# Performance work log

Hardware: AMD Instinct MI355X
Metric: run time of the kernel (lower is better)

The kernel has to match this reference:

```python
import jax, jax.numpy as jnp
import numpy as np
from jax import lax

B, L, F, H, K = 16, 512, 384, 384, 3
MAX_OUT = 4096  # static upper bound on sum of durations (L * (fill_max-1) = 3584)
EPS = 1e-5
PAD = K // 2


def setup_inputs() -> dict:
    key = jax.random.key(0)
    ks = jax.random.split(key, 6)
    s = 0.02
    return {
        "input": jax.random.normal(ks[0], (B, L, F), jnp.float32),
        "target": jax.random.randint(ks[1], (B, L), 0, 8, jnp.int32),
        "conv1_w": jax.random.normal(ks[2], (H, F, K), jnp.float32) * s,
        "conv1_b": jnp.zeros((H,), jnp.float32),
        "ln1_g": jnp.ones((H,), jnp.float32),
        "ln1_b": jnp.zeros((H,), jnp.float32),
        "conv2_w": jax.random.normal(ks[3], (F, H, K), jnp.float32) * s,
        "conv2_b": jnp.zeros((F,), jnp.float32),
        "ln2_g": jnp.ones((F,), jnp.float32),
        "ln2_b": jnp.zeros((F,), jnp.float32),
        "lin_w": jax.random.normal(ks[4], (F, 1), jnp.float32) * s,
        "lin_b": jnp.zeros((1,), jnp.float32),
    }


def _conv1d(x, w, b):
    # x: [B, L, Cin] -> [B, L, Cout]; w: [Cout, Cin, K] (torch Conv1d layout)
    y = lax.conv_general_dilated(
        x.transpose(0, 2, 1), w, window_strides=(1,), padding=[(PAD, PAD)],
        dimension_numbers=("NCH", "OIH", "NCH"))
    return y.transpose(0, 2, 1) + b


def _layer_norm(x, g, b):
    mu = jnp.mean(x, axis=-1, keepdims=True)
    var = jnp.mean(jnp.square(x - mu), axis=-1, keepdims=True)
    return (x - mu) * lax.rsqrt(var + EPS) * g + b


def _length_regulate(x, dur_int):
    # cumsum-based index mapping + gather (vectorized LR_function)
    ends = jnp.cumsum(dur_int, axis=-1)                      # [B, L]
    ts = jnp.arange(MAX_OUT)                                 # [T]
    idx = jax.vmap(lambda e: jnp.searchsorted(e, ts, side="right"))(ends)  # [B, T]
    gathered = jnp.take_along_axis(x, jnp.clip(idx, 0, L - 1)[:, :, None], axis=1)
    mask = (ts[None, :] < ends[:, -1:]).astype(x.dtype)      # zero-pad past total length
    return gathered * mask[:, :, None]


def reference(input, target, conv1_w, conv1_b, ln1_g, ln1_b,
              conv2_w, conv2_b, ln2_g, ln2_b, lin_w, lin_b):
    # DurationPredictor (eval mode: dropout is identity)
    h = jax.nn.relu(_layer_norm(_conv1d(input, conv1_w, conv1_b), ln1_g, ln1_b))
    h = jax.nn.relu(_layer_norm(_conv1d(h, conv2_w, conv2_b), ln2_g, ln2_b))
    durations = jnp.exp(jax.nn.relu(h @ lin_w + lin_b))       # [B, L, 1]
    # LR_function with target durations (round of int target is identity)
    out = _length_regulate(input, target)                      # [B, MAX_OUT, F]
    return out, durations
```

## Files before the change

kernel.cpp:

```cpp
#include <hip/hip_runtime.h>
#include <math.h>

#define B_ 16
#define L_ 512
#define F_ 384
#define H_ 384
#define K_ 3
#define MAX_OUT_ 4096
#define EPS_ 1e-5f

#define M_TOTAL (B_ * L_)
#define KDIM (K_ * F_)
#define NMB 128
#define NCG 6
#define NST 36
#define APANEL (66 * 64)
#define AMBLK (12 * APANEL)
#define APLANE (NMB * AMBLK)
#define BSTEP 4096
#define BCG (NST * BSTEP)
#define BPLANE (NCG * BCG)

typedef __attribute__((ext_vector_type(8))) short bf16x8;
typedef __attribute__((ext_vector_type(4))) float f32x4;

__device__ inline unsigned short bf16_rne(float v) {
    unsigned int u = __float_as_uint(v);
    unsigned int r = (u + 0x7fffu + ((u >> 16) & 1u)) >> 16;
    return (unsigned short)r;
}
__device__ inline void bf16_split(float v, unsigned short& hi, unsigned short& lo) {
    hi = bf16_rne(v);
    float hf = __uint_as_float(((unsigned int)hi) << 16);
    lo = bf16_rne(v - hf);
}

__global__ void k_scan_idx(const int* __restrict__ target, int* __restrict__ idx) {
    __shared__ int e[L_];
    const int b = blockIdx.x;
    const int tid = threadIdx.x;
    e[tid] = target[b * L_ + tid];
    __syncthreads();
    for (int off = 1; off < L_; off <<= 1) {
        int add = (tid >= off) ? e[tid - off] : 0;
        __syncthreads();
        e[tid] += add;
        __syncthreads();
    }
    const int total = e[L_ - 1];
    for (int t = tid; t < MAX_OUT_; t += L_) {
        int lo = 0, hi = L_;
        while (lo < hi) {
            int m = (lo + hi) >> 1;
            if (e[m] <= t) lo = m + 1; else hi = m;
        }
        int v = (t < total) ? min(lo, L_ - 1) : -1;
        idx[b * MAX_OUT_ + t] = v;
    }
}

__global__ void k_prep(const float* __restrict__ x,
                       const float* __restrict__ w1, const float* __restrict__ w2,
                       unsigned short* __restrict__ aph, unsigned short* __restrict__ apl,
                       unsigned short* __restrict__ b1h, unsigned short* __restrict__ b1l,
                       unsigned short* __restrict__ b2h, unsigned short* __restrict__ b2l) {
    const int NA8 = NMB * 12 * 66 * 4;
    const int NB8 = NCG * NST * 64 * 4;
    const int total = NA8 + 2 * NB8;
    for (int i = blockIdx.x * blockDim.x + threadIdx.x; i < total;
         i += gridDim.x * blockDim.x) {
        if (i < NA8) {
            const int m = i / 3168;
            int r1 = i - m * 3168;
            const int fs = r1 / 264;
            int r2 = r1 - fs * 264;
            const int rp = r2 >> 2;
            const int p = r2 & 3;
            const int cgk = p ^ ((rp >> 1) & 3);
            const int f0 = fs * 32 + cgk * 8;
            const int ll = ((m & 7) << 6) + rp - 1;
            ushort4 h0 = {0,0,0,0}, h1 = {0,0,0,0}, l0 = {0,0,0,0}, l1 = {0,0,0,0};
            if (ll >= 0 && ll < L_) {
                const float* src = x + ((size_t)((m >> 3) * L_ + ll) * F_ + f0);
                float4 va = ((const float4*)src)[0];
                float4 vb = ((const float4*)src)[1];
                bf16_split(va.x, h0.x, l0.x); bf16_split(va.y, h0.y, l0.y);
                bf16_split(va.z, h0.z, l0.z); bf16_split(va.w, h0.w, l0.w);
                bf16_split(vb.x, h1.x, l1.x); bf16_split(vb.y, h1.y, l1.y);
                bf16_split(vb.z, h1.z, l1.z); bf16_split(vb.w, h1.w, l1.w);
            }
            ((ushort4*)aph)[i * 2] = h0;  ((ushort4*)aph)[i * 2 + 1] = h1;
            ((ushort4*)apl)[i * 2] = l0;  ((ushort4*)apl)[i * 2 + 1] = l1;
        } else {
            int j = i - NA8;
            const int conv = j / NB8;
            int j2 = j - conv * NB8;
            const float* w = conv ? w2 : w1;
            unsigned short* bh = conv ? b2h : b1h;
            unsigned short* bl = conv ? b2l : b1l;
            const int cg = j2 / 9216;
            int r1 = j2 - cg * 9216;
            const int s = r1 / 256;
            int r2 = r1 - s * 256;
            const int rc = r2 >> 2;
            const int p = r2 & 3;
            const int tap = s / 12;
            const int fs = s - tap * 12;
            const int cgk = p ^ ((rc >> 1) & 3);
            const int f0 = fs * 32 + cgk * 8;
            const int h = cg * 64 + rc;
            ushort4 hv0, hv1, lv0, lv1;
            unsigned short th, tl;
#define WSPLIT(E, DH, DL) bf16_split(w[(size_t)(h * F_ + f0 + (E)) * K_ + tap], th, tl); DH = th; DL = tl;
            WSPLIT(0, hv0.x, lv0.x) WSPLIT(1, hv0.y, lv0.y)
            WSPLIT(2, hv0.z, lv0.z) WSPLIT(3, hv0.w, lv0.w)
            WSPLIT(4, hv1.x, lv1.x) WSPLIT(5, hv1.y, lv1.y)
            WSPLIT(6, hv1.z, lv1.z) WSPLIT(7, hv1.w, lv1.w)
#undef WSPLIT
            ((ushort4*)bh)[j2 * 2] = hv0;  ((ushort4*)bh)[j2 * 2 + 1] = hv1;
            ((ushort4*)bl)[j2 * 2] = lv0;  ((ushort4*)bl)[j2 * 2 + 1] = lv1;
        }
    }
}

typedef __attribute__((address_space(3))) char lds_char;
typedef const __attribute__((address_space(1))) char g_char;

#define GLDS(gsrc, ldst)                                                   \
    __builtin_amdgcn_global_load_lds((g_char*)(gsrc), (lds_char*)(ldst), 16, 0, 0)

#define ST(S) {                                                            \
    const int off = wvA ? ((((S) % 12) * 66 + (S) / 12) * 64) : ((S) * 4096); \
    _Pragma("unroll")                                                      \
    for (int q = 0; q < 4; ++q)                                            \
        GLDS(srcbase + off + q * 1024,                                     \
             smem + ((S) % 3) * 16384 + wvoff + q * 1024);                 \
}

#define MFMA1(A, Bv, MI, NI)                                               \
    acc[MI][NI] = __builtin_amdgcn_mfma_f32_16x16x32_bf16(A, Bv, acc[MI][NI], 0, 0, 0);

#define STEP(S, NW, DOSTAGE) {                                             \
    asm volatile("s_waitcnt vmcnt(" #NW ")" ::: "memory");                 \
    __builtin_amdgcn_s_barrier();                                          \
    const char* bb = smem + ((S) % 3) * 16384;                             \
    const int tp = (S) / 12;                                               \
    bf16x8 ah0 = *(const bf16x8*)(bb + aadr0[tp]);                         \
    bf16x8 ah1 = *(const bf16x8*)(bb + aadr1[tp]);                         \
    bf16x8 al0 = *(const bf16x8*)(bb + 4096 + aadr0[tp]);                  \
    bf16x8 al1 = *(const bf16x8*)(bb + 4096 + aadr1[tp]);                  \
    bf16x8 bh0 = *(const bf16x8*)(bb + 8192 + badr0);                      \
    bf16x8 bh1 = *(const bf16x8*)(bb + 8192 + badr1);                      \
    bf16x8 bl0 = *(const bf16x8*)(bb + 12288 + badr0);                     \
    bf16x8 bl1 = *(const bf16x8*)(bb + 12288 + badr1);                     \
    asm volatile("s_waitcnt lgkmcnt(0)" ::: "memory");                     \
    __builtin_amdgcn_sched_barrier(0);                                     \
    __builtin_amdgcn_s_barrier();                                          \
    DOSTAGE;                                                               \
    __builtin_amdgcn_s_setprio(1);                                         \
    MFMA1(ah0, bh0, 0, 0) MFMA1(ah0, bh1, 0, 1)                            \
    MFMA1(ah1, bh0, 1, 0) MFMA1(ah1, bh1, 1, 1)                            \
    MFMA1(ah0, bl0, 0, 0) MFMA1(ah0, bl1, 0, 1)                            \
    MFMA1(ah1, bl0, 1, 0) MFMA1(ah1, bl1, 1, 1)                            \
    MFMA1(al0, bh0, 0, 0) MFMA1(al0, bh1, 0, 1)                            \
    MFMA1(al1, bh0, 1, 0) MFMA1(al1, bh1, 1, 1)                            \
    __builtin_amdgcn_s_setprio(0);                                         \
}

__global__ __launch_bounds__(256, 3) void k_gemm(
        const unsigned short* __restrict__ Aph,
        const unsigned short* __restrict__ Apl,
        const unsigned short* __restrict__ Bph,
        const unsigned short* __restrict__ Bpl,
        float* __restrict__ C) {
    __shared__ __align__(1024) char smem[49152];
    const int lane = threadIdx.x & 63;
    const int wv = threadIdx.x >> 6;
    const int wr = wv >> 1;
    const int wc = wv & 1;
    const int m = blockIdx.x;
    const int cg = blockIdx.y;
    const int r0 = m * 64;
    const int h0 = cg * 64;

    const bool wvA = (wv < 2);
    const int wvoff = wv * 4096;
    const char* srcbase;
    {
        const char* ap = (wv == 0) ? (const char*)Aph : (const char*)Apl;
        const char* bp = (wv == 2) ? (const char*)Bph : (const char*)Bpl;
        srcbase = (wvA ? ap + (size_t)m * AMBLK : bp + (size_t)cg * BCG) + lane * 16;
    }

    const int fr = lane & 15;
    const int fc = lane >> 4;
    const int rowA0 = wr * 32 + fr, rowA1 = rowA0 + 16;
    const int colB0 = wc * 32 + fr, colB1 = colB0 + 16;
    int aadr0[3], aadr1[3];
#pragma unroll
    for (int t = 0; t < 3; ++t) {
        aadr0[t] = rowA0 * 64 + ((fc ^ (((rowA0 + t) >> 1) & 3)) << 4);
        aadr1[t] = rowA1 * 64 + ((fc ^ (((rowA1 + t) >> 1) & 3)) << 4);
    }
    const int badr0 = colB0 * 64 + ((fc ^ ((colB0 >> 1) & 3)) << 4);
    const int badr1 = colB1 * 64 + ((fc ^ ((colB1 >> 1) & 3)) << 4);

    const f32x4 z4 = {0.f, 0.f, 0.f, 0.f};
    f32x4 acc[2][2];
    acc[0][0] = z4; acc[0][1] = z4; acc[1][0] = z4; acc[1][1] = z4;

    ST(0) ST(1) ST(2)

    STEP(0, 8, ST(3))   STEP(1, 8, ST(4))   STEP(2, 8, ST(5))
    STEP(3, 8, ST(6))   STEP(4, 8, ST(7))   STEP(5, 8, ST(8))
    STEP(6, 8, ST(9))   STEP(7, 8, ST(10))  STEP(8, 8, ST(11))
    STEP(9, 8, ST(12))  STEP(10, 8, ST(13)) STEP(11, 8, ST(14))
    STEP(12, 8, ST(15)) STEP(13, 8, ST(16)) STEP(14, 8, ST(17))
    STEP(15, 8, ST(18)) STEP(16, 8, ST(19)) STEP(17, 8, ST(20))
    STEP(18, 8, ST(21)) STEP(19, 8, ST(22)) STEP(20, 8, ST(23))
    STEP(21, 8, ST(24)) STEP(22, 8, ST(25)) STEP(23, 8, ST(26))
    STEP(24, 8, ST(27)) STEP(25, 8, ST(28)) STEP(26, 8, ST(29))
    STEP(27, 8, ST(30)) STEP(28, 8, ST(31)) STEP(29, 8, ST(32))
    STEP(30, 8, ST(33)) STEP(31, 8, ST(34)) STEP(32, 8, ST(35))
    STEP(33, 8, )       STEP(34, 4, )       STEP(35, 0, )

    const int rb = (lane >> 4) * 4;
#pragma unroll
    for (int mi = 0; mi < 2; ++mi)
#pragma unroll
        for (int ni = 0; ni < 2; ++ni)
#pragma unroll
            for (int r = 0; r < 4; ++r)
                C[(size_t)(r0 + wr * 32 + mi * 16 + rb + r) * H_ +
                  h0 + wc * 32 + ni * 16 + fr] = acc[mi][ni][r];
}

__global__ __launch_bounds__(256) void k_lnrelu(
        const float* __restrict__ c, const float* __restrict__ cb,
        const float* __restrict__ g, const float* __restrict__ bt,
        unsigned short* __restrict__ oh, unsigned short* __restrict__ ol) {
    const int row = blockIdx.x * 4 + (threadIdx.x >> 6);
    const int lane = threadIdx.x & 63;
    const float* cr = c + (size_t)row * H_;
    float2 dv[3];
    dv[0] = ((const float2*)cr)[lane];
    dv[1] = ((const float2*)cr)[lane + 64];
    dv[2] = ((const float2*)cr)[lane + 128];
#pragma unroll
    for (int p = 0; p < 3; ++p) {
        const int ch = 2 * (lane + 64 * p);
        dv[p].x += cb[ch];
        dv[p].y += cb[ch + 1];
    }
    float s = dv[0].x + dv[0].y + dv[1].x + dv[1].y + dv[2].x + dv[2].y;
    float s2 = dv[0].x * dv[0].x + dv[0].y * dv[0].y + dv[1].x * dv[1].x
             + dv[1].y * dv[1].y + dv[2].x * dv[2].x + dv[2].y * dv[2].y;
    for (int off = 32; off >= 1; off >>= 1) {
        s += __shfl_xor(s, off);
        s2 += __shfl_xor(s2, off);
    }
    const float mu = s * (1.f / H_);
    const float var = s2 * (1.f / H_) - mu * mu;
    const float rs = rsqrtf(var + EPS_);
    unsigned short hv[6], lv[6];
#pragma unroll
    for (int p = 0; p < 3; ++p) {
        const int ch = 2 * (lane + 64 * p);
        float r0 = fmaxf((dv[p].x - mu) * rs * g[ch] + bt[ch], 0.f);
        float r1 = fmaxf((dv[p].y - mu) * rs * g[ch + 1] + bt[ch + 1], 0.f);
        bf16_split(r0, hv[2 * p], lv[2 * p]);
        bf16_split(r1, hv[2 * p + 1], lv[2 * p + 1]);
    }
#define WSLOT(M, RP) {                                                        \
    _Pragma("unroll")                                                         \
    for (int p = 0; p < 3; ++p) {                                             \
        const int ch = 2 * (lane + 64 * p);                                   \
        const int fs = ch >> 5;                                               \
        const int k32 = ch & 31;                                              \
        const int pst = (k32 >> 3) ^ (((RP) >> 1) & 3);                       \
        const size_t ix = ((size_t)(((M) * 12 + fs) * 66 + (RP)) * 4 + pst) * 8 + (k32 & 7); \
        *(ushort2*)(oh + ix) = make_ushort2(hv[2 * p], hv[2 * p + 1]);        \
        *(ushort2*)(ol + ix) = make_ushort2(lv[2 * p], lv[2 * p + 1]);        \
    }                                                                         \
}
    const int m1 = row >> 6;
    const int rsub = row & 63;
    WSLOT(m1, rsub + 1);
    if (rsub == 0 && (row & 511) != 0)   WSLOT(m1 - 1, 65);
    if (rsub == 63 && (row & 511) != 511) WSLOT(m1 + 1, 0);
#undef WSLOT
}

__global__ __launch_bounds__(256) void k_fin(
        const float* __restrict__ c, const float* __restrict__ cb,
        const float* __restrict__ g, const float* __restrict__ bt,
        const float* __restrict__ lw, const float* __restrict__ lb,
        float* __restrict__ dur) {
    const int row = blockIdx.x * 4 + (threadIdx.x >> 6);
    const int lane = threadIdx.x & 63;
    const float* cr = c + (size_t)row * F_;
    float2 dv[3];
    dv[0] = ((const float2*)cr)[lane];
    dv[1] = ((const float2*)cr)[lane + 64];
    dv[2] = ((const float2*)cr)[lane + 128];
#pragma unroll
    for (int p = 0; p < 3; ++p) {
        const int ch = 2 * (lane + 64 * p);
        dv[p].x += cb[ch];
        dv[p].y += cb[ch + 1];
    }
    float s = dv[0].x + dv[0].y + dv[1].x + dv[1].y + dv[2].x + dv[2].y;
    float s2 = dv[0].x * dv[0].x + dv[0].y * dv[0].y + dv[1].x * dv[1].x
             + dv[1].y * dv[1].y + dv[2].x * dv[2].x + dv[2].y * dv[2].y;
    for (int off = 32; off >= 1; off >>= 1) {
        s += __shfl_xor(s, off);
        s2 += __shfl_xor(s2, off);
    }
    const float mu = s * (1.f / F_);
    const float var = s2 * (1.f / F_) - mu * mu;
    const float rs = rsqrtf(var + EPS_);
    float dot = 0.f;
#pragma unroll
    for (int p = 0; p < 3; ++p) {
        const int ch = 2 * (lane + 64 * p);
        float r0 = fmaxf((dv[p].x - mu) * rs * g[ch] + bt[ch], 0.f);
        float r1 = fmaxf((dv[p].y - mu) * rs * g[ch + 1] + bt[ch + 1], 0.f);
        dot += r0 * lw[ch] + r1 * lw[ch + 1];
    }
    for (int off = 32; off >= 1; off >>= 1) dot += __shfl_xor(dot, off);
    if (lane == 0) dur[row] = expf(fmaxf(dot + lb[0], 0.f));
}

__global__ void k_gather(const float4* __restrict__ x, const int* __restrict__ idx,
                         float4* __restrict__ out) {
    const int F4 = F_ / 4;
    const int total = B_ * MAX_OUT_ * F4;
    for (int i = blockIdx.x * blockDim.x + threadIdx.x; i < total;
         i += gridDim.x * blockDim.x) {
        int row = i / F4;
        int f4 = i - row * F4;
        int t = row % MAX_OUT_;
        int b = row / MAX_OUT_;
        int id = idx[b * MAX_OUT_ + t];
        float4 v = make_float4(0.f, 0.f, 0.f, 0.f);
        if (id >= 0) v = x[((size_t)b * L_ + id) * F4 + f4];
        out[i] = v;
    }
}

extern "C" void kernel_launch(void* const* d_in, const int* in_sizes, int n_in,
                              void* d_out, int out_size, void* d_ws, size_t ws_size,
                              hipStream_t stream) {
    const float* input   = (const float*)d_in[0];
    const int*   target  = (const int*)d_in[1];
    const float* conv1_w = (const float*)d_in[2];
    const float* conv1_b = (const float*)d_in[3];
    const float* ln1_g   = (const float*)d_in[4];
    const float* ln1_b   = (const float*)d_in[5];
    const float* conv2_w = (const float*)d_in[6];
    const float* conv2_b = (const float*)d_in[7];
    const float* ln2_g   = (const float*)d_in[8];
    const float* ln2_b   = (const float*)d_in[9];
    const float* lin_w   = (const float*)d_in[10];
    const float* lin_b   = (const float*)d_in[11];

    float* out0 = (float*)d_out;
    float* dur  = out0 + (size_t)B_ * MAX_OUT_ * F_;
    float* c    = out0;
    char* ob = (char*)d_out;
    unsigned short* aph = (unsigned short*)(ob + (16u << 20));
    unsigned short* apl = (unsigned short*)(ob + (24u << 20));

    char* ws = (char*)d_ws;
    int* idx = (int*)ws;
    unsigned short* b1h = (unsigned short*)(ws + 262144);
    unsigned short* b1l = b1h + BPLANE / 2;
    unsigned short* b2h = b1l + BPLANE / 2;
    unsigned short* b2l = b2h + BPLANE / 2;

    hipLaunchKernelGGL(k_scan_idx, dim3(B_), dim3(L_), 0, stream, target, idx);
    hipLaunchKernelGGL(k_prep, dim3(2048), dim3(256), 0, stream,
                       input, conv1_w, conv2_w, aph, apl, b1h, b1l, b2h, b2l);
    hipLaunchKernelGGL(k_gemm, dim3(NMB, NCG), dim3(256), 0, stream,
                       aph, apl, b1h, b1l, c);
    hipLaunchKernelGGL(k_lnrelu, dim3(M_TOTAL / 4), dim3(256), 0, stream,
                       c, conv1_b, ln1_g, ln1_b, aph, apl);
    hipLaunchKernelGGL(k_gemm, dim3(NMB, NCG), dim3(256), 0, stream,
                       aph, apl, b2h, b2l, c);
    hipLaunchKernelGGL(k_fin, dim3(M_TOTAL / 4), dim3(256), 0, stream,
                       c, conv2_b, ln2_g, ln2_b, lin_w, lin_b, dur);
    hipLaunchKernelGGL(k_gather, dim3(4096), dim3(256), 0, stream,
                       (const float4*)input, idx, (float4*)out0);
}
```

Measured before the change: 101.8 us.

## Load GEMM B operand directly into registers with double-buffered prefetch

The B (weight) fragments are no longer staged through LDS. Each wave loads its B fragments straight from global memory into registers, prefetching one stage ahead with alternating X/Y register sets. All four waves now share the A-tile staging through LDS, two async global-to-LDS loads each, which halves the shared-memory footprint and removes LDS traffic for B. In exchange it adds register pressure and relies on global/L2 latency for the B loads, with hand-tuned vmcnt wait counts that must match the new mix of outstanding loads.

```diff
diff --git a/kernel.cpp b/kernel.cpp
--- a/kernel.cpp
+++ b/kernel.cpp
@@ -130,40 +130,44 @@
     __builtin_amdgcn_global_load_lds((g_char*)(gsrc), (lds_char*)(ldst), 16, 0, 0)
 
 #define ST(S) {                                                            \
-    const int off = wvA ? ((((S) % 12) * 66 + (S) / 12) * 64) : ((S) * 4096); \
-    _Pragma("unroll")                                                      \
-    for (int q = 0; q < 4; ++q)                                            \
-        GLDS(srcbase + off + q * 1024,                                     \
-             smem + ((S) % 3) * 16384 + wvoff + q * 1024);                 \
+    const int offp = (((S) % 12) * 66 + (S) / 12) * 64;                    \
+    GLDS(asrc0 + offp, smem + ((S) % 3) * 8192 + dst0);                    \
+    GLDS(asrc1 + offp, smem + ((S) % 3) * 8192 + dst1);                    \
+}
+
+#define LDB(S, R) {                                                        \
+    R##h0 = *(const bf16x8*)(bsrch + (S) * 4096 + badr0);                  \
+    R##h1 = *(const bf16x8*)(bsrch + (S) * 4096 + badr1);                  \
+    R##l0 = *(const bf16x8*)(bsrcl + (S) * 4096 + badr0);                  \
+    R##l1 = *(const bf16x8*)(bsrcl + (S) * 4096 + badr1);                  \
 }
 
 #define MFMA1(A, Bv, MI, NI)                                               \
     acc[MI][NI] = __builtin_amdgcn_mfma_f32_16x16x32_bf16(A, Bv, acc[MI][NI], 0, 0, 0);
 
-#define STEP(S, NW, DOSTAGE) {                                             \
-    asm volatile("s_waitcnt vmcnt(" #NW ")" ::: "memory");                 \
+#define SB __builtin_amdgcn_sched_barrier(0)
+
+#define STEP(S, KA, DOST, DOLDB, BH0, BH1, BL0, BL1) {                     \
+    asm volatile("s_waitcnt vmcnt(" #KA ")" ::: "memory");                 \
     __builtin_amdgcn_s_barrier();                                          \
-    const char* bb = smem + ((S) % 3) * 16384;                             \
-    const int tp = (S) / 12;                                               \
-    bf16x8 ah0 = *(const bf16x8*)(bb + aadr0[tp]);                         \
-    bf16x8 ah1 = *(const bf16x8*)(bb + aadr1[tp]);                         \
-    bf16x8 al0 = *(const bf16x8*)(bb + 4096 + aadr0[tp]);                  \
-    bf16x8 al1 = *(const bf16x8*)(bb + 4096 + aadr1[tp]);                  \
-    bf16x8 bh0 = *(const bf16x8*)(bb + 8192 + badr0);                      \
-    bf16x8 bh1 = *(const bf16x8*)(bb + 8192 + badr1);                      \
-    bf16x8 bl0 = *(const bf16x8*)(bb + 12288 + badr0);                     \
-    bf16x8 bl1 = *(const bf16x8*)(bb + 12288 + badr1);                     \
+    const char* bb = smem + ((S) % 3) * 8192;                              \
+    bf16x8 ah0 = *(const bf16x8*)(bb + aadr0[(S) / 12]);                   \
+    bf16x8 ah1 = *(const bf16x8*)(bb + aadr1[(S) / 12]);                   \
+    bf16x8 al0 = *(const bf16x8*)(bb + 4096 + aadr0[(S) / 12]);            \
+    bf16x8 al1 = *(const bf16x8*)(bb + 4096 + aadr1[(S) / 12]);            \
     asm volatile("s_waitcnt lgkmcnt(0)" ::: "memory");                     \
-    __builtin_amdgcn_sched_barrier(0);                                     \
+    SB;                                                                    \
     __builtin_amdgcn_s_barrier();                                          \
-    DOSTAGE;                                                               \
+    DOST;                                                                  \
+    DOLDB;                                                                 \
+    SB;                                                                    \
     __builtin_amdgcn_s_setprio(1);                                         \
-    MFMA1(ah0, bh0, 0, 0) MFMA1(ah0, bh1, 0, 1)                            \
-    MFMA1(ah1, bh0, 1, 0) MFMA1(ah1, bh1, 1, 1)                            \
-    MFMA1(ah0, bl0, 0, 0) MFMA1(ah0, bl1, 0, 1)                            \
-    MFMA1(ah1, bl0, 1, 0) MFMA1(ah1, bl1, 1, 1)                            \
-    MFMA1(al0, bh0, 0, 0) MFMA1(al0, bh1, 0, 1)                            \
-    MFMA1(al1, bh0, 1, 0) MFMA1(al1, bh1, 1, 1)                            \
+    MFMA1(ah0, BH0, 0, 0) MFMA1(ah0, BH1, 0, 1)                            \
+    MFMA1(ah1, BH0, 1, 0) MFMA1(ah1, BH1, 1, 1)                            \
+    MFMA1(ah0, BL0, 0, 0) MFMA1(ah0, BL1, 0, 1)                            \
+    MFMA1(ah1, BL0, 1, 0) MFMA1(ah1, BL1, 1, 1)                            \
+    MFMA1(al0, BH0, 0, 0) MFMA1(al0, BH1, 0, 1)                            \
+    MFMA1(al1, BH0, 1, 0) MFMA1(al1, BH1, 1, 1)                            \
     __builtin_amdgcn_s_setprio(0);                                         \
 }
 
@@ -173,7 +177,7 @@
         const unsigned short* __restrict__ Bph,
         const unsigned short* __restrict__ Bpl,
         float* __restrict__ C) {
-    __shared__ __align__(1024) char smem[49152];
+    __shared__ __align__(1024) char smem[24576];
     const int lane = threadIdx.x & 63;
     const int wv = threadIdx.x >> 6;
     const int wr = wv >> 1;
@@ -183,14 +187,16 @@
     const int r0 = m * 64;
     const int h0 = cg * 64;
 
-    const bool wvA = (wv < 2);
-    const int wvoff = wv * 4096;
-    const char* srcbase;
-    {
-        const char* ap = (wv == 0) ? (const char*)Aph : (const char*)Apl;
-        const char* bp = (wv == 2) ? (const char*)Bph : (const char*)Bpl;
-        srcbase = (wvA ? ap + (size_t)m * AMBLK : bp + (size_t)cg * BCG) + lane * 16;
-    }
+    const char* aplane = (const char*)((wv < 2) ? Aph : Apl)
+                         + (size_t)m * AMBLK + lane * 16;
+    const int cid = (wv & 1) * 2;
+    const char* asrc0 = aplane + cid * 1024;
+    const char* asrc1 = aplane + (cid + 1) * 1024;
+    const int dst0 = ((wv < 2) ? 0 : 4096) + cid * 1024;
+    const int dst1 = dst0 + 1024;
+
+    const char* bsrch = (const char*)Bph + (size_t)cg * BCG;
+    const char* bsrcl = (const char*)Bpl + (size_t)cg * BCG;
 
     const int fr = lane & 15;
     const int fc = lane >> 4;
@@ -209,20 +215,48 @@
     f32x4 acc[2][2];
     acc[0][0] = z4; acc[0][1] = z4; acc[1][0] = z4; acc[1][1] = z4;
 
+    bf16x8 Xh0, Xh1, Xl0, Xl1, Yh0, Yh1, Yl0, Yl1;
+
     ST(0) ST(1) ST(2)
-
-    STEP(0, 8, ST(3))   STEP(1, 8, ST(4))   STEP(2, 8, ST(5))
-    STEP(3, 8, ST(6))   STEP(4, 8, ST(7))   STEP(5, 8, ST(8))
-    STEP(6, 8, ST(9))   STEP(7, 8, ST(10))  STEP(8, 8, ST(11))
-    STEP(9, 8, ST(12))  STEP(10, 8, ST(13)) STEP(11, 8, ST(14))
-    STEP(12, 8, ST(15)) STEP(13, 8, ST(16)) STEP(14, 8, ST(17))
-    STEP(15, 8, ST(18)) STEP(16, 8, ST(19)) STEP(17, 8, ST(20))
-    STEP(18, 8, ST(21)) STEP(19, 8, ST(22)) STEP(20, 8, ST(23))
-    STEP(21, 8, ST(24)) STEP(22, 8, ST(25)) STEP(23, 8, ST(26))
-    STEP(24, 8, ST(27)) STEP(25, 8, ST(28)) STEP(26, 8, ST(29))
-    STEP(27, 8, ST(30)) STEP(28, 8, ST(31)) STEP(29, 8, ST(32))
-    STEP(30, 8, ST(33)) STEP(31, 8, ST(34)) STEP(32, 8, ST(35))
-    STEP(33, 8, )       STEP(34, 4, )       STEP(35, 0, )
+    LDB(0, X)
+    SB;
+
+    STEP(0,  8,  ST(3),  LDB(1, Y),  Xh0, Xh1, Xl0, Xl1)
+    STEP(1,  12, ST(4),  LDB(2, X),  Yh0, Yh1, Yl0, Yl1)
+    STEP(2,  16, ST(5),  LDB(3, Y),  Xh0, Xh1, Xl0, Xl1)
+    STEP(3,  16, ST(6),  LDB(4, X),  Yh0, Yh1, Yl0, Yl1)
+    STEP(4,  16, ST(7),  LDB(5, Y),  Xh0, Xh1, Xl0, Xl1)
+    STEP(5,  16, ST(8),  LDB(6, X),  Yh0, Yh1, Yl0, Yl1)
+    STEP(6,  16, ST(9),  LDB(7, Y),  Xh0, Xh1, Xl0, Xl1)
+    STEP(7,  16, ST(10), LDB(8, X),  Yh0, Yh1, Yl0, Yl1)
+    STEP(8,  16, ST(11), LDB(9, Y),  Xh0, Xh1, Xl0, Xl1)
+    STEP(9,  16, ST(12), LDB(10, X), Yh0, Yh1, Yl0, Yl1)
+    STEP(10, 16, ST(13), LDB(11, Y), Xh0, Xh1, Xl0, Xl1)
+    STEP(11, 16, ST(14), LDB(12, X), Yh0, Yh1, Yl0, Yl1)
+    STEP(12, 16, ST(15), LDB(13, Y), Xh0, Xh1, Xl0, Xl1)
+    STEP(13, 16, ST(16), LDB(14, X), Yh0, Yh1, Yl0, Yl1)
+    STEP(14, 16, ST(17), LDB(15, Y), Xh0, Xh1, Xl0, Xl1)
+    STEP(15, 16, ST(18), LDB(16, X), Yh0, Yh1, Yl0, Yl1)
+    STEP(16, 16, ST(19), LDB(17, Y), Xh0, Xh1, Xl0, Xl1)
+    STEP(17, 16, ST(20), LDB(18, X), Yh0, Yh1, Yl0, Yl1)
+    STEP(18, 16, ST(21), LDB(19, Y), Xh0, Xh1, Xl0, Xl1)
+    STEP(19, 16, ST(22), LDB(20, X), Yh0, Yh1, Yl0, Yl1)
+    STEP(20, 16, ST(23), LDB(21, Y), Xh0, Xh1, Xl0, Xl1)
+    STEP(21, 16, ST(24), LDB(22, X), Yh0, Yh1, Yl0, Yl1)
+    STEP(22, 16, ST(25), LDB(23, Y), Xh0, Xh1, Xl0, Xl1)
+    STEP(23, 16, ST(26), LDB(24, X), Yh0, Yh1, Yl0, Yl1)
+    STEP(24, 16, ST(27), LDB(25, Y), Xh0, Xh1, Xl0, Xl1)
+    STEP(25, 16, ST(28), LDB(26, X), Yh0, Yh1, Yl0, Yl1)
+    STEP(26, 16, ST(29), LDB(27, Y), Xh0, Xh1, Xl0, Xl1)
+    STEP(27, 16, ST(30), LDB(28, X), Yh0, Yh1, Yl0, Yl1)
+    STEP(28, 16, ST(31), LDB(29, Y), Xh0, Xh1, Xl0, Xl1)
+    STEP(29, 16, ST(32), LDB(30, X), Yh0, Yh1, Yl0, Yl1)
+    STEP(30, 16, ST(33), LDB(31, Y), Xh0, Xh1, Xl0, Xl1)
+    STEP(31, 16, ST(34), LDB(32, X), Yh0, Yh1, Yl0, Yl1)
+    STEP(32, 16, ST(35), LDB(33, Y), Xh0, Xh1, Xl0, Xl1)
+    STEP(33, 16, (void)0, LDB(34, X), Yh0, Yh1, Yl0, Yl1)
+    STEP(34, 14, (void)0, LDB(35, Y), Xh0, Xh1, Xl0, Xl1)
+    STEP(35, 12, (void)0, (void)0,    Yh0, Yh1, Yl0, Yl1)
 
     const int rb = (lane >> 4) * 4;
 #pragma unroll
```

Measured after the change: 107.2 us. 5.3% more time.

## Fuse scan with prep and final LN with gather; retime GEMM pipeline

Applied to the files above, without the earlier changes.

Merges the index scan into the prep kernel and the final layernorm/duration step into the gather kernel. This removes two launches, and the c buffer moves to workspace so gather output no longer aliases it. The GEMM loop now prefetches two stages ahead instead of three. It also issues the next stage's global loads before waiting on LDS reads and drops the second barrier per step. That cuts synchronisation, but dropping the barrier with a 3-slot ring at distance two may risk a write-after-read race on shared memory.

```diff
diff --git a/kernel.cpp b/kernel.cpp
--- a/kernel.cpp
+++ b/kernel.cpp
@@ -35,40 +35,41 @@
     lo = bf16_rne(v - hf);
 }
 
-__global__ void k_scan_idx(const int* __restrict__ target, int* __restrict__ idx) {
-    __shared__ int e[L_];
-    const int b = blockIdx.x;
-    const int tid = threadIdx.x;
-    e[tid] = target[b * L_ + tid];
-    __syncthreads();
-    for (int off = 1; off < L_; off <<= 1) {
-        int add = (tid >= off) ? e[tid - off] : 0;
+__global__ void k_scan_prep(const int* __restrict__ target, int* __restrict__ idx,
+                            const float* __restrict__ x,
+                            const float* __restrict__ w1, const float* __restrict__ w2,
+                            unsigned short* __restrict__ aph, unsigned short* __restrict__ apl,
+                            unsigned short* __restrict__ b1h, unsigned short* __restrict__ b1l,
+                            unsigned short* __restrict__ b2h, unsigned short* __restrict__ b2l) {
+    if (blockIdx.x < 16) {
+        __shared__ int e[L_];
+        const int b = blockIdx.x;
+        const int tid = threadIdx.x;
+        e[tid] = target[b * L_ + tid];
         __syncthreads();
-        e[tid] += add;
-        __syncthreads();
-    }
-    const int total = e[L_ - 1];
-    for (int t = tid; t < MAX_OUT_; t += L_) {
-        int lo = 0, hi = L_;
-        while (lo < hi) {
-            int m = (lo + hi) >> 1;
-            if (e[m] <= t) lo = m + 1; else hi = m;
-        }
-        int v = (t < total) ? min(lo, L_ - 1) : -1;
-        idx[b * MAX_OUT_ + t] = v;
-    }
-}
-
-__global__ void k_prep(const float* __restrict__ x,
-                       const float* __restrict__ w1, const float* __restrict__ w2,
-                       unsigned short* __restrict__ aph, unsigned short* __restrict__ apl,
-                       unsigned short* __restrict__ b1h, unsigned short* __restrict__ b1l,
-                       unsigned short* __restrict__ b2h, unsigned short* __restrict__ b2l) {
+        for (int off = 1; off < L_; off <<= 1) {
+            int add = (tid >= off) ? e[tid - off] : 0;
+            __syncthreads();
+            e[tid] += add;
+            __syncthreads();
+        }
+        const int total = e[L_ - 1];
+        for (int t = tid; t < MAX_OUT_; t += L_) {
+            int lo = 0, hi = L_;
+            while (lo < hi) {
+                int m = (lo + hi) >> 1;
+                if (e[m] <= t) lo = m + 1; else hi = m;
+            }
+            int v = (t < total) ? min(lo, L_ - 1) : -1;
+            idx[b * MAX_OUT_ + t] = v;
+        }
+        return;
+    }
     const int NA8 = NMB * 12 * 66 * 4;
     const int NB8 = NCG * NST * 64 * 4;
     const int total = NA8 + 2 * NB8;
-    for (int i = blockIdx.x * blockDim.x + threadIdx.x; i < total;
-         i += gridDim.x * blockDim.x) {
+    for (int i = (blockIdx.x - 16) * blockDim.x + threadIdx.x; i < total;
+         i += (gridDim.x - 16) * blockDim.x) {
         if (i < NA8) {
             const int m = i / 3168;
             int r1 = i - m * 3168;
@@ -153,10 +154,9 @@
     bf16x8 bh1 = *(const bf16x8*)(bb + 8192 + badr1);                      \
     bf16x8 bl0 = *(const bf16x8*)(bb + 12288 + badr0);                     \
     bf16x8 bl1 = *(const bf16x8*)(bb + 12288 + badr1);                     \
+    DOSTAGE;                                                               \
     asm volatile("s_waitcnt lgkmcnt(0)" ::: "memory");                     \
     __builtin_amdgcn_sched_barrier(0);                                     \
-    __builtin_amdgcn_s_barrier();                                          \
-    DOSTAGE;                                                               \
     __builtin_amdgcn_s_setprio(1);                                         \
     MFMA1(ah0, bh0, 0, 0) MFMA1(ah0, bh1, 0, 1)                            \
     MFMA1(ah1, bh0, 1, 0) MFMA1(ah1, bh1, 1, 1)                            \
@@ -209,20 +209,20 @@
     f32x4 acc[2][2];
     acc[0][0] = z4; acc[0][1] = z4; acc[1][0] = z4; acc[1][1] = z4;
 
-    ST(0) ST(1) ST(2)
-
-    STEP(0, 8, ST(3))   STEP(1, 8, ST(4))   STEP(2, 8, ST(5))
-    STEP(3, 8, ST(6))   STEP(4, 8, ST(7))   STEP(5, 8, ST(8))
-    STEP(6, 8, ST(9))   STEP(7, 8, ST(10))  STEP(8, 8, ST(11))
-    STEP(9, 8, ST(12))  STEP(10, 8, ST(13)) STEP(11, 8, ST(14))
-    STEP(12, 8, ST(15)) STEP(13, 8, ST(16)) STEP(14, 8, ST(17))
-    STEP(15, 8, ST(18)) STEP(16, 8, ST(19)) STEP(17, 8, ST(20))
-    STEP(18, 8, ST(21)) STEP(19, 8, ST(22)) STEP(20, 8, ST(23))
-    STEP(21, 8, ST(24)) STEP(22, 8, ST(25)) STEP(23, 8, ST(26))
-    STEP(24, 8, ST(27)) STEP(25, 8, ST(28)) STEP(26, 8, ST(29))
-    STEP(27, 8, ST(30)) STEP(28, 8, ST(31)) STEP(29, 8, ST(32))
-    STEP(30, 8, ST(33)) STEP(31, 8, ST(34)) STEP(32, 8, ST(35))
-    STEP(33, 8, )       STEP(34, 4, )       STEP(35, 0, )
+    ST(0) ST(1)
+
+    STEP(0, 4, ST(2))   STEP(1, 4, ST(3))   STEP(2, 4, ST(4))
+    STEP(3, 4, ST(5))   STEP(4, 4, ST(6))   STEP(5, 4, ST(7))
+    STEP(6, 4, ST(8))   STEP(7, 4, ST(9))   STEP(8, 4, ST(10))
+    STEP(9, 4, ST(11))  STEP(10, 4, ST(12)) STEP(11, 4, ST(13))
+    STEP(12, 4, ST(14)) STEP(13, 4, ST(15)) STEP(14, 4, ST(16))
+    STEP(15, 4, ST(17)) STEP(16, 4, ST(18)) STEP(17, 4, ST(19))
+    STEP(18, 4, ST(20)) STEP(19, 4, ST(21)) STEP(20, 4, ST(22))
+    STEP(21, 4, ST(23)) STEP(22, 4, ST(24)) STEP(23, 4, ST(25))
+    STEP(24, 4, ST(26)) STEP(25, 4, ST(27)) STEP(26, 4, ST(28))
+    STEP(27, 4, ST(29)) STEP(28, 4, ST(30)) STEP(29, 4, ST(31))
+    STEP(30, 4, ST(32)) STEP(31, 4, ST(33)) STEP(32, 4, ST(34))
+    STEP(33, 4, ST(35)) STEP(34, 4, )       STEP(35, 0, )
 
     const int rb = (lane >> 4) * 4;
 #pragma unroll
@@ -291,48 +291,48 @@
 #undef WSLOT
 }
 
-__global__ __launch_bounds__(256) void k_fin(
+__global__ __launch_bounds__(256) void k_fin_gather(
         const float* __restrict__ c, const float* __restrict__ cb,
         const float* __restrict__ g, const float* __restrict__ bt,
         const float* __restrict__ lw, const float* __restrict__ lb,
-        float* __restrict__ dur) {
-    const int row = blockIdx.x * 4 + (threadIdx.x >> 6);
-    const int lane = threadIdx.x & 63;
-    const float* cr = c + (size_t)row * F_;
-    float2 dv[3];
-    dv[0] = ((const float2*)cr)[lane];
-    dv[1] = ((const float2*)cr)[lane + 64];
-    dv[2] = ((const float2*)cr)[lane + 128];
-#pragma unroll
-    for (int p = 0; p < 3; ++p) {
-        const int ch = 2 * (lane + 64 * p);
-        dv[p].x += cb[ch];
-        dv[p].y += cb[ch + 1];
-    }
-    float s = dv[0].x + dv[0].y + dv[1].x + dv[1].y + dv[2].x + dv[2].y;
-    float s2 = dv[0].x * dv[0].x + dv[0].y * dv[0].y + dv[1].x * dv[1].x
-             + dv[1].y * dv[1].y + dv[2].x * dv[2].x + dv[2].y * dv[2].y;
-    for (int off = 32; off >= 1; off >>= 1) {
-        s += __shfl_xor(s, off);
-        s2 += __shfl_xor(s2, off);
-    }
-    const float mu = s * (1.f / F_);
-    const float var = s2 * (1.f / F_) - mu * mu;
-    const float rs = rsqrtf(var + EPS_);
-    float dot = 0.f;
-#pragma unroll
-    for (int p = 0; p < 3; ++p) {
-        const int ch = 2 * (lane + 64 * p);
-        float r0 = fmaxf((dv[p].x - mu) * rs * g[ch] + bt[ch], 0.f);
-        float r1 = fmaxf((dv[p].y - mu) * rs * g[ch + 1] + bt[ch + 1], 0.f);
-        dot += r0 * lw[ch] + r1 * lw[ch + 1];
-    }
-    for (int off = 32; off >= 1; off >>= 1) dot += __shfl_xor(dot, off);
-    if (lane == 0) dur[row] = expf(fmaxf(dot + lb[0], 0.f));
-}
-
-__global__ void k_gather(const float4* __restrict__ x, const int* __restrict__ idx,
-                         float4* __restrict__ out) {
+        float* __restrict__ dur,
+        const float4* __restrict__ x, const int* __restrict__ idx,
+        float4* __restrict__ out) {
+    if (blockIdx.x < 2048) {
+        const int row = blockIdx.x * 4 + (threadIdx.x >> 6);
+        const int lane = threadIdx.x & 63;
+        const float* cr = c + (size_t)row * F_;
+        float2 dv[3];
+        dv[0] = ((const float2*)cr)[lane];
+        dv[1] = ((const float2*)cr)[lane + 64];
+        dv[2] = ((const float2*)cr)[lane + 128];
+#pragma unroll
+        for (int p = 0; p < 3; ++p) {
+            const int ch = 2 * (lane + 64 * p);
+            dv[p].x += cb[ch];
+            dv[p].y += cb[ch + 1];
+        }
+        float s = dv[0].x + dv[0].y + dv[1].x + dv[1].y + dv[2].x + dv[2].y;
+        float s2 = dv[0].x * dv[0].x + dv[0].y * dv[0].y + dv[1].x * dv[1].x
+                 + dv[1].y * dv[1].y + dv[2].x * dv[2].x + dv[2].y * dv[2].y;
+        for (int off = 32; off >= 1; off >>= 1) {
+            s += __shfl_xor(s, off);
+            s2 += __shfl_xor(s2, off);
+        }
+        const float mu = s * (1.f / F_);
+        const float var = s2 * (1.f / F_) - mu * mu;
+        const float rs = rsqrtf(var + EPS_);
+        float dot = 0.f;
+#pragma unroll
+        for (int p = 0; p < 3; ++p) {
+            const int ch = 2 * (lane + 64 * p);
+            float r0 = fmaxf((dv[p].x - mu) * rs * g[ch] + bt[ch], 0.f);
+            float r1 = fmaxf((dv[p].y - mu) * rs * g[ch + 1] + bt[ch + 1], 0.f);
+            dot += r0 * lw[ch] + r1 * lw[ch + 1];
+        }
+        for (int off = 32; off >= 1; off >>= 1) dot += __shfl_xor(dot, off);
+        if (lane == 0) dur[row] = expf(fmaxf(dot + lb[0], 0.f));
+    }
     const int F4 = F_ / 4;
     const int total = B_ * MAX_OUT_ * F4;
     for (int i = blockIdx.x * blockDim.x + threadIdx.x; i < total;
@@ -366,7 +366,6 @@
 
     float* out0 = (float*)d_out;
     float* dur  = out0 + (size_t)B_ * MAX_OUT_ * F_;
-    float* c    = out0;
     char* ob = (char*)d_out;
     unsigned short* aph = (unsigned short*)(ob + (16u << 20));
     unsigned short* apl = (unsigned short*)(ob + (24u << 20));
@@ -377,18 +376,18 @@
     unsigned short* b1l = b1h + BPLANE / 2;
     unsigned short* b2h = b1l + BPLANE / 2;
     unsigned short* b2l = b2h + BPLANE / 2;
-
-    hipLaunchKernelGGL(k_scan_idx, dim3(B_), dim3(L_), 0, stream, target, idx);
-    hipLaunchKernelGGL(k_prep, dim3(2048), dim3(256), 0, stream,
-                       input, conv1_w, conv2_w, aph, apl, b1h, b1l, b2h, b2l);
+    float* c = (float*)(ws + 262144 + 4 * (size_t)BPLANE);
+
+    hipLaunchKernelGGL(k_scan_prep, dim3(1040), dim3(512), 0, stream,
+                       target, idx, input, conv1_w, conv2_w,
+                       aph, apl, b1h, b1l, b2h, b2l);
     hipLaunchKernelGGL(k_gemm, dim3(NMB, NCG), dim3(256), 0, stream,
                        aph, apl, b1h, b1l, c);
     hipLaunchKernelGGL(k_lnrelu, dim3(M_TOTAL / 4), dim3(256), 0, stream,
                        c, conv1_b, ln1_g, ln1_b, aph, apl);
     hipLaunchKernelGGL(k_gemm, dim3(NMB, NCG), dim3(256), 0, stream,
                        aph, apl, b2h, b2l, c);
-    hipLaunchKernelGGL(k_fin, dim3(M_TOTAL / 4), dim3(256), 0, stream,
-                       c, conv2_b, ln2_g, ln2_b, lin_w, lin_b, dur);
-    hipLaunchKernelGGL(k_gather, dim3(4096), dim3(256), 0, stream,
+    hipLaunchKernelGGL(k_fin_gather, dim3(4096), dim3(256), 0, stream,
+                       c, conv2_b, ln2_g, ln2_b, lin_w, lin_b, dur,
                        (const float4*)input, idx, (float4*)out0);
 }
```

After: 89.88 us. -11.7%, faster.
